# Performance work log

Measured on AMD Instinct MI355X. Metric: run time of the kernel, lower is better.

## Reference

```python
import jax, jax.numpy as jnp
import numpy as np

N_HEAD = 16
HEAD_DIM = 64
EPS_RMS = 1e-6


def _rope(x, cos, sin):
    # x: [B, T, H, D]; cos/sin: [T, D//2] broadcast to [1, T, 1, D//2]
    d2 = x.shape[-1] // 2
    x1, x2 = x[..., :d2], x[..., d2:]
    c = cos[None, :, None, :]
    s = sin[None, :, None, :]
    return jnp.concatenate([x1 * c + x2 * s, -x1 * s + x2 * c], axis=-1)


def _rms_norm(x):
    return x * jax.lax.rsqrt(jnp.mean(x * x, axis=-1, keepdims=True) + EPS_RMS)


def setup_inputs() -> dict:
    key = jax.random.key(0)
    ks = jax.random.split(key, 7)
    B, T, C = 1, 4096, 1024
    x = jax.random.normal(ks[0], (B, T, C), dtype=jnp.float32)
    # realistic rotary angles
    d2 = HEAD_DIM // 2
    inv_freq = 1.0 / (10000.0 ** (np.arange(0, d2, dtype=np.float32) / d2))
    ang = np.arange(T, dtype=np.float32)[:, None] * inv_freq[None, :]
    cos = jnp.asarray(np.cos(ang), dtype=jnp.float32)
    sin = jnp.asarray(np.sin(ang), dtype=jnp.float32)
    scale = 0.02
    wq = jax.random.normal(ks[1], (C, C), dtype=jnp.float32) * scale
    wk = jax.random.normal(ks[2], (C, C), dtype=jnp.float32) * scale
    wv = jax.random.normal(ks[3], (C, C), dtype=jnp.float32) * scale
    wproj = jax.random.normal(ks[4], (C, C), dtype=jnp.float32) * scale
    return {"x": x, "cos": cos, "sin": sin, "wq": wq, "wk": wk, "wv": wv, "wproj": wproj}


def reference(x, cos, sin, wq, wk, wv, wproj):
    B, T, C = x.shape
    H, D = N_HEAD, HEAD_DIM
    # QKV projections (torch Linear: x @ W.T)
    q = (x @ wq.T).reshape(B, T, H, D)
    k = (x @ wk.T).reshape(B, T, H, D)
    v = (x @ wv.T).reshape(B, T, H, D)
    # RoPE then QK RMS-norm
    q = _rms_norm(_rope(q, cos, sin))
    k = _rms_norm(_rope(k, cos, sin))
    # [B, H, T, D]
    q = q.transpose(0, 2, 1, 3)
    k = k.transpose(0, 2, 1, 3)
    v = v.transpose(0, 2, 1, 3)
    scores = jnp.einsum('bhqd,bhkd->bhqk', q, k) * (1.0 / D ** 0.5)
    # causal mask (kv_cache is None, Tq == Tk == T)
    mask = jnp.tril(jnp.ones((T, T), dtype=bool))
    scores = jnp.where(mask[None, None, :, :], scores, -jnp.inf)
    attn = jax.nn.sigmoid(scores)  # sigmoid(-inf) == 0
    y = jnp.einsum('bhqk,bhkd->bhqd', attn, v)
    y = y / (T ** 0.5 + 1e-6)
    y = y.transpose(0, 2, 1, 3).reshape(B, T, C)
    return y @ wproj.T
```

## Files before the change

### kernel.cpp

```cpp
#include <hip/hip_runtime.h>

typedef __attribute__((ext_vector_type(8))) short bf16x8;
typedef __attribute__((ext_vector_type(4))) float f32x4;
typedef __attribute__((ext_vector_type(16))) float f32x16;

__device__ inline f32x4 mfma16(bf16x8 a, bf16x8 b, f32x4 c) {
    return __builtin_amdgcn_mfma_f32_16x16x32_bf16(a, b, c, 0, 0, 0);
}
__device__ inline f32x16 mfma32(bf16x8 a, bf16x8 b, f32x16 c) {
    return __builtin_amdgcn_mfma_f32_32x32x16_bf16(a, b, c, 0, 0, 0);
}

__device__ inline short f2bf(float f) {
    unsigned u = __builtin_bit_cast(unsigned, f);
    unsigned r = (u + 0x7fffu + ((u >> 16) & 1u)) >> 16;
    return (short)r;
}
__device__ inline float bf2f(short h) {
    unsigned u = ((unsigned)(unsigned short)h) << 16;
    return __builtin_bit_cast(float, u);
}

__device__ inline unsigned cvt_pk_bf16(float lo, float hi) {
    unsigned r;
    asm("v_cvt_pk_bf16_f32 %0, %1, %2" : "=v"(r) : "v"(lo), "v"(hi));
    return r;
}
__device__ inline void plane_swap(unsigned& a, unsigned& b) {
    asm("v_permlane32_swap_b32 %0, %1" : "+v"(a), "+v"(b));
}
__device__ inline float exp2_hw(float x) {
    float r;
    asm("v_exp_f32 %0, %1" : "=v"(r) : "v"(x));
    return r;
}

#define GAS(p) (const __attribute__((address_space(1))) void*)(p)
#define LAS(p) (__attribute__((address_space(3))) void*)(p)

#define T_SEQ 4096
#define C_DIM 1024
#define N_HEAD 16
#define HEAD_DIM 64
#define QSCALE (-0.18033688011112042f)
#define INV64 (1.0f / (64.0f + 1e-6f))

__global__ __launch_bounds__(256) void cast5(
    const float* __restrict__ s0, const float* __restrict__ s1,
    const float* __restrict__ s2, const float* __restrict__ s3,
    const float* __restrict__ s4,
    short* __restrict__ d0, short* __restrict__ d1, short* __restrict__ d2,
    short* __restrict__ d3, short* __restrict__ d4,
    int n0, int n1, int n2, int n3, int n4)
{
    int z = blockIdx.y;
    const float* s; short* d; int n;
    switch (z) {
        case 0: s = s0; d = d0; n = n0; break;
        case 1: s = s1; d = d1; n = n1; break;
        case 2: s = s2; d = d2; n = n2; break;
        case 3: s = s3; d = d3; n = n3; break;
        default: s = s4; d = d4; n = n4; break;
    }
    float sc = (z == 4) ? INV64 : 1.0f;
    int i = (blockIdx.x * 256 + threadIdx.x) * 4;
    if (i >= n) return;
    float4 v = *(const float4*)&s[i];
    short4 o;
    o.x = f2bf(v.x * sc); o.y = f2bf(v.y * sc);
    o.z = f2bf(v.z * sc); o.w = f2bf(v.w * sc);
    *(short4*)&d[i] = o;
}

#define QSTAGE(t_, b_) do {                                                      \
    int k0_ = (t_) * 32;                                                         \
    _Pragma("unroll")                                                            \
    for (int s2_ = 0; s2_ < 2; s2_++) {                                          \
        int rbase_ = wave * 32 + s2_ * 16;                                       \
        __builtin_amdgcn_global_load_lds(                                        \
            GAS(&A[(size_t)(row0 + rbase_ + srow) * KK + k0_ + scolx]),          \
            LAS(&sA[b_][rbase_ * 32]), 16, 0, 0);                                \
        __builtin_amdgcn_global_load_lds(                                        \
            GAS(&B[(size_t)(col0 + rbase_ + srow) * KK + k0_ + scolx]),          \
            LAS(&sB[b_][rbase_ * 32]), 16, 0, 0);                                \
    }                                                                            \
} while (0)

#define GEMM_STEP2(t_, nt_, bcur_) do {                                          \
    if ((t_) + 1 < (nt_)) {                                                      \
        QSTAGE((t_) + 1, (bcur_) ^ 1);                                           \
        asm volatile("s_waitcnt vmcnt(4)" ::: "memory");                         \
    } else {                                                                     \
        asm volatile("s_waitcnt vmcnt(0)" ::: "memory");                         \
    }                                                                            \
    __builtin_amdgcn_s_barrier();                                                \
    bf16x8 af[4], bfv[4];                                                        \
    _Pragma("unroll")                                                            \
    for (int m = 0; m < 4; m++) {                                                \
        int row_ = wr * 64 + m * 16 + llo;                                       \
        af[m] = *(const bf16x8*)&sA[bcur_][row_ * 32 + ((lhi ^ (llo & 3)) * 8)]; \
    }                                                                            \
    _Pragma("unroll")                                                            \
    for (int n = 0; n < 4; n++) {                                                \
        int row_ = wc * 64 + n * 16 + llo;                                       \
        bfv[n] = *(const bf16x8*)&sB[bcur_][row_ * 32 + ((lhi ^ (llo & 3)) * 8)];\
    }                                                                            \
    __builtin_amdgcn_s_setprio(1);                                               \
    _Pragma("unroll")                                                            \
    for (int m = 0; m < 4; m++)                                                  \
        _Pragma("unroll")                                                        \
        for (int n = 0; n < 4; n++)                                              \
            acc[m][n] = mfma16(af[m], bfv[n], acc[m][n]);                        \
    __builtin_amdgcn_s_setprio(0);                                               \
    asm volatile("" ::: "memory");                                               \
    __builtin_amdgcn_s_barrier();                                                \
} while (0)

__global__ __launch_bounds__(256, 4) void gemm_qkv(
    const short* __restrict__ A,
    const short* __restrict__ B0, const short* __restrict__ B1,
    const short* __restrict__ B2,
    short* __restrict__ qnb, short* __restrict__ knb, short* __restrict__ vtb,
    const float* __restrict__ cosT, const float* __restrict__ sinT)
{
    int xx = blockIdx.x;
    int ct = xx & 7, z = xx >> 3;
    const short* B = (z == 0) ? B0 : ((z == 1) ? B1 : B2);

    __shared__ alignas(16) short sA[2][128 * 32];
    __shared__ alignas(16) short sB[2][128 * 32];

    int tid  = threadIdx.x;
    int wave = tid >> 6, lane = tid & 63;
    int lhi  = lane >> 4, llo = lane & 15;
    int wr   = wave >> 1, wc = wave & 1;
    int row0 = blockIdx.y * 128, col0 = ct * 128;
    const int KK = C_DIM;

    int srow  = lane >> 2;
    int scolx = (((lane & 3) ^ (srow & 3)) * 8);

    f32x4 acc[4][4];
#pragma unroll
    for (int m = 0; m < 4; m++)
#pragma unroll
        for (int n = 0; n < 4; n++)
            acc[m][n] = (f32x4){0.f, 0.f, 0.f, 0.f};

    QSTAGE(0, 0);
    int bcur = 0;
    for (int t = 0; t < 32; t++) {
        GEMM_STEP2(t, 32, bcur);
        bcur ^= 1;
    }

    int hH = ct * 2 + wc;
    if (z < 2) {
        short* dst = z ? knb : qnb;
        float osc = z ? 1.0f : QSCALE;
#pragma unroll
        for (int m = 0; m < 4; m++)
#pragma unroll
            for (int r = 0; r < 4; r++) {
                int row = row0 + wr * 64 + m * 16 + lhi * 4 + r;
                float c0 = cosT[row * 32 + llo],      c1 = cosT[row * 32 + 16 + llo];
                float s0 = sinT[row * 32 + llo],      s1 = sinT[row * 32 + 16 + llo];
                float e0 = acc[m][0][r], e1 = acc[m][1][r];
                float e2 = acc[m][2][r], e3 = acc[m][3][r];
                float r0 = e0 * c0 + e2 * s0;
                float r1 = e1 * c1 + e3 * s1;
                float r2 = e2 * c0 - e0 * s0;
                float r3 = e3 * c1 - e1 * s1;
                float sq = r0 * r0 + r1 * r1 + r2 * r2 + r3 * r3;
                sq += __shfl_xor(sq, 1);
                sq += __shfl_xor(sq, 2);
                sq += __shfl_xor(sq, 4);
                sq += __shfl_xor(sq, 8);
                float inv = rsqrtf(sq * (1.0f / 64.0f) + 1e-6f) * osc;
                size_t base = ((size_t)hH * T_SEQ + row) * HEAD_DIM + llo;
                dst[base +  0] = f2bf(r0 * inv);
                dst[base + 16] = f2bf(r1 * inv);
                dst[base + 32] = f2bf(r2 * inv);
                dst[base + 48] = f2bf(r3 * inv);
            }
    } else {
#pragma unroll
        for (int m = 0; m < 4; m++)
#pragma unroll
            for (int n = 0; n < 4; n++) {
                int trow = row0 + wr * 64 + m * 16 + lhi * 4;
                short4 o;
                o.x = f2bf(acc[m][n][0]);
                o.y = f2bf(acc[m][n][1]);
                o.z = f2bf(acc[m][n][2]);
                o.w = f2bf(acc[m][n][3]);
                *(short4*)&vtb[((size_t)(hH * HEAD_DIM + n * 16 + llo)) * T_SEQ + trow] = o;
            }
    }
}

__global__ __launch_bounds__(256, 4) void gemm_proj(
    const short* __restrict__ A, const short* __restrict__ B,
    float* __restrict__ C, int M, int N, int K)
{
    __shared__ alignas(16) short sA[2][128 * 32];
    __shared__ alignas(16) short sB[2][128 * 32];

    int tid  = threadIdx.x;
    int wave = tid >> 6, lane = tid & 63;
    int lhi  = lane >> 4, llo = lane & 15;
    int wr   = wave >> 1, wc = wave & 1;
    int row0 = blockIdx.y * 128, col0 = blockIdx.x * 128;
    const int KK = K;

    int srow  = lane >> 2;
    int scolx = (((lane & 3) ^ (srow & 3)) * 8);

    f32x4 acc[4][4];
#pragma unroll
    for (int m = 0; m < 4; m++)
#pragma unroll
        for (int n = 0; n < 4; n++)
            acc[m][n] = (f32x4){0.f, 0.f, 0.f, 0.f};

    int nt = K >> 5;
    QSTAGE(0, 0);
    int bcur = 0;
    for (int t = 0; t < nt; t++) {
        GEMM_STEP2(t, nt, bcur);
        bcur ^= 1;
    }

#pragma unroll
    for (int m = 0; m < 4; m++)
#pragma unroll
        for (int n = 0; n < 4; n++)
#pragma unroll
            for (int r = 0; r < 4; r++) {
                int row = row0 + wr * 64 + m * 16 + lhi * 4 + r;
                int col = col0 + wc * 64 + n * 16 + llo;
                C[(size_t)row * N + col] = acc[m][n][r];
            }
}

#define STAGE6(s_, bf_) do {                                                     \
    int kb_ = (s_) * 64;                                                         \
    int r_  = lane >> 3;                                                         \
    int ss_ = (lane & 7) ^ r_;                                                   \
    __builtin_amdgcn_global_load_lds(                                            \
        GAS(Kh + (size_t)(kb_ + wv * 16 + r_) * HEAD_DIM + ss_ * 8),             \
        LAS(Smem + (bf_) * 8192 + (wv * 16) * 128), 16, 0, 0);                   \
    __builtin_amdgcn_global_load_lds(                                            \
        GAS(Kh + (size_t)(kb_ + wv * 16 + 8 + r_) * HEAD_DIM + ss_ * 8),         \
        LAS(Smem + (bf_) * 8192 + (wv * 16 + 8) * 128), 16, 0, 0);               \
    __builtin_amdgcn_global_load_lds(                                            \
        GAS(Vh + (size_t)(wv * 16 + r_) * T_SEQ + kb_ + ss_ * 8),                \
        LAS(Smem + 16384 + (bf_) * 8192 + (wv * 16) * 128), 16, 0, 0);           \
    __builtin_amdgcn_global_load_lds(                                            \
        GAS(Vh + (size_t)(wv * 16 + 8 + r_) * T_SEQ + kb_ + ss_ * 8),            \
        LAS(Smem + 16384 + (bf_) * 8192 + (wv * 16 + 8) * 128), 16, 0, 0);       \
} while (0)

__global__ __launch_bounds__(256, 4) void attn6(
    const short* __restrict__ qn, const short* __restrict__ kn,
    const short* __restrict__ vt, short* __restrict__ yb)
{
    __shared__ alignas(16) char Smem[32768];

    int id = blockIdx.x;
    int h  = id & 15;
    int g  = id >> 4;
    int t  = (g < 16) ? (63 - g) : (g < 32) ? (g - 16)
           : (g < 48) ? (79 - g) : (g - 32);
    int ns = t + 1;

    int tid = threadIdx.x, wv = tid >> 6, lane = tid & 63;
    int lo = lane & 31, hi = lane >> 5;
    int band = wv & 1, tm = wv >> 1;

    const short* Qh = qn + (size_t)h * T_SEQ * HEAD_DIM;
    const short* Kh = kn + (size_t)h * T_SEQ * HEAD_DIM;
    const short* Vh = vt + (size_t)h * HEAD_DIM * T_SEQ;

    int q0 = t * 64;
    int qrow  = q0 + band * 32 + lo;
    int qmaxw = q0 + band * 32 + 31;

    const short* Qr = &Qh[(size_t)qrow * HEAD_DIM + hi * 8];
    bf16x8 qf0 = *(const bf16x8*)&Qr[0];
    bf16x8 qf1 = *(const bf16x8*)&Qr[16];
    bf16x8 qf2 = *(const bf16x8*)&Qr[32];
    bf16x8 qf3 = *(const bf16x8*)&Qr[48];

    f32x16 zed;
#pragma unroll
    for (int r = 0; r < 16; r++) zed[r] = 0.f;

    f32x16 yac0, yac1;
#pragma unroll
    for (int r = 0; r < 16; r++) { yac0[r] = 0.f; yac1[r] = 0.f; }

    unsigned sw   = (unsigned)((lo & 7) << 4);
    unsigned krow = (unsigned)((tm * 32 + lo) * 128);
    unsigned ko0 = krow + ((0u * 32 + hi * 16) ^ sw);
    unsigned ko1 = krow + ((1u * 32 + hi * 16) ^ sw);
    unsigned ko2 = krow + ((2u * 32 + hi * 16) ^ sw);
    unsigned ko3 = krow + ((3u * 32 + hi * 16) ^ sw);
    unsigned vrow0 = (unsigned)(lo * 128)        + 16384u;
    unsigned vrow1 = (unsigned)((32 + lo) * 128) + 16384u;
    unsigned vo00 = vrow0 + (((unsigned)(tm * 64 + 0 * 32 + hi * 16)) ^ sw);
    unsigned vo01 = vrow0 + (((unsigned)(tm * 64 + 1 * 32 + hi * 16)) ^ sw);
    unsigned vo10 = vrow1 + (((unsigned)(tm * 64 + 0 * 32 + hi * 16)) ^ sw);
    unsigned vo11 = vrow1 + (((unsigned)(tm * 64 + 1 * 32 + hi * 16)) ^ sw);

    STAGE6(0, 0);
    int buf = 0;
    for (int s = 0; s < ns; s++) {
        if (s + 1 < ns) {
            STAGE6(s + 1, buf ^ 1);
            asm volatile("s_waitcnt vmcnt(4)" ::: "memory");
        } else {
            asm volatile("s_waitcnt vmcnt(0)" ::: "memory");
        }
        __builtin_amdgcn_s_barrier();

        int kb0 = s * 64 + tm * 32;
        if (kb0 <= qmaxw) {
            const char* B_ = Smem + (buf << 13);
            bf16x8 kf0 = *(const bf16x8*)(B_ + ko0);
            bf16x8 kf1 = *(const bf16x8*)(B_ + ko1);
            bf16x8 kf2 = *(const bf16x8*)(B_ + ko2);
            bf16x8 kf3 = *(const bf16x8*)(B_ + ko3);
            bf16x8 vf00 = *(const bf16x8*)(B_ + vo00);
            bf16x8 vf01 = *(const bf16x8*)(B_ + vo01);
            bf16x8 vf10 = *(const bf16x8*)(B_ + vo10);
            bf16x8 vf11 = *(const bf16x8*)(B_ + vo11);

            f32x16 sv;
            __builtin_amdgcn_s_setprio(1);
            sv = mfma32(kf0, qf0, zed);
            sv = mfma32(kf1, qf1, sv);
            sv = mfma32(kf2, qf2, sv);
            sv = mfma32(kf3, qf3, sv);
            __builtin_amdgcn_s_setprio(0);

            if (kb0 + 31 > q0 + band * 32) {
#pragma unroll
                for (int r = 0; r < 16; r++) {
                    int kvg = kb0 + (r & 3) + 8 * (r >> 2) + 4 * hi;
                    float pv = __builtin_amdgcn_rcpf(1.f + exp2_hw(sv[r]));
                    sv[r] = (kvg <= qrow) ? pv : 0.f;
                }
            } else {
#pragma unroll
                for (int r = 0; r < 16; r++)
                    sv[r] = __builtin_amdgcn_rcpf(1.f + exp2_hw(sv[r]));
            }

#pragma unroll
            for (int k2 = 0; k2 < 2; k2++) {
                unsigned wA = cvt_pk_bf16(sv[8 * k2 + 0], sv[8 * k2 + 1]);
                unsigned wC = cvt_pk_bf16(sv[8 * k2 + 2], sv[8 * k2 + 3]);
                unsigned wB = cvt_pk_bf16(sv[8 * k2 + 4], sv[8 * k2 + 5]);
                unsigned wD = cvt_pk_bf16(sv[8 * k2 + 6], sv[8 * k2 + 7]);
                plane_swap(wA, wB);
                plane_swap(wC, wD);
                union { unsigned u[4]; bf16x8 v; } pw;
                pw.u[0] = wA; pw.u[1] = wC; pw.u[2] = wB; pw.u[3] = wD;
                __builtin_amdgcn_s_setprio(1);
                yac0 = mfma32(pw.v, k2 ? vf01 : vf00, yac0);
                yac1 = mfma32(pw.v, k2 ? vf11 : vf10, yac1);
                __builtin_amdgcn_s_setprio(0);
            }
        }
        asm volatile("" ::: "memory");
        __builtin_amdgcn_s_barrier();
        buf ^= 1;
    }

    __syncthreads();
    float* Yred = (float*)Smem;
    if (tm == 1) {
#pragma unroll
        for (int d = 0; d < 2; d++)
#pragma unroll
            for (int r = 0; r < 16; r++) {
                int crow = (r & 3) + 8 * (r >> 2) + 4 * hi;
                Yred[(band * 32 + crow) * 64 + d * 32 + lo] = d ? yac1[r] : yac0[r];
            }
    }
    __syncthreads();
    if (tm == 0) {
#pragma unroll
        for (int d = 0; d < 2; d++)
#pragma unroll
            for (int r = 0; r < 16; r++) {
                int crow = (r & 3) + 8 * (r >> 2) + 4 * hi;
                float v = (d ? yac1[r] : yac0[r]) + Yred[(band * 32 + crow) * 64 + d * 32 + lo];
                yb[(size_t)(q0 + band * 32 + crow) * C_DIM + h * HEAD_DIM + d * 32 + lo] = f2bf(v);
            }
    }
}

extern "C" void kernel_launch(void* const* d_in, const int* in_sizes, int n_in,
                              void* d_out, int out_size, void* d_ws, size_t ws_size,
                              hipStream_t stream)
{
    const float* x    = (const float*)d_in[0];
    const float* cosT = (const float*)d_in[1];
    const float* sinT = (const float*)d_in[2];
    const float* wq   = (const float*)d_in[3];
    const float* wk   = (const float*)d_in[4];
    const float* wv   = (const float*)d_in[5];
    const float* wp   = (const float*)d_in[6];

    char* ws = (char*)d_ws;
    const size_t MB = 1024 * 1024;
    short* xb    = (short*)(ws + 0);
    short* wqb   = (short*)(ws + 8  * MB);
    short* wkb   = (short*)(ws + 10 * MB);
    short* wvb   = (short*)(ws + 12 * MB);
    short* wpb   = (short*)(ws + 14 * MB);
    short* qnb   = (short*)(ws + 16 * MB);
    short* knb   = (short*)(ws + 24 * MB);
    short* vtb   = (short*)(ws + 32 * MB);
    short* yb    = (short*)(ws + 40 * MB);

    cast5<<<dim3(4096, 5, 1), 256, 0, stream>>>(
        x, wq, wk, wv, wp, xb, wqb, wkb, wvb, wpb,
        T_SEQ * C_DIM, C_DIM * C_DIM, C_DIM * C_DIM, C_DIM * C_DIM, C_DIM * C_DIM);

    gemm_qkv<<<dim3(24, 32, 1), 256, 0, stream>>>(
        xb, wqb, wkb, wvb, qnb, knb, vtb, cosT, sinT);

    attn6<<<1024, 256, 0, stream>>>(qnb, knb, vtb, yb);

    gemm_proj<<<dim3(8, 32, 1), 256, 0, stream>>>(
        yb, wpb, (float*)d_out, T_SEQ, C_DIM, C_DIM);
}
```

Before: 129.1 us.

## Triple-buffer K/V tiles in attention with one barrier per step

Moves the attention kernel's K/V staging from a double buffer to a triple buffer, prefetching two tiles ahead and unrolling the loop three times with fixed buffer indices. This lets each step use a single barrier instead of two. The goal is to hide more global-load latency and cut synchronisation cost. In exchange LDS per block grows to 48KB and the occupancy bound drops from 4 to 3 blocks per CU.

```diff
diff --git a/kernel.cpp b/kernel.cpp
--- a/kernel.cpp
+++ b/kernel.cpp
@@ -243,7 +243,8 @@
             }
 }
 
-#define STAGE6(s_, bf_) do {                                                     \
+
+#define STAGE20(s_, bf_) do {                                                    \
     int kb_ = (s_) * 64;                                                         \
     int r_  = lane >> 3;                                                         \
     int ss_ = (lane & 7) ^ r_;                                                   \
@@ -255,17 +256,70 @@
         LAS(Smem + (bf_) * 8192 + (wv * 16 + 8) * 128), 16, 0, 0);               \
     __builtin_amdgcn_global_load_lds(                                            \
         GAS(Vh + (size_t)(wv * 16 + r_) * T_SEQ + kb_ + ss_ * 8),                \
-        LAS(Smem + 16384 + (bf_) * 8192 + (wv * 16) * 128), 16, 0, 0);           \
+        LAS(Smem + 24576 + (bf_) * 8192 + (wv * 16) * 128), 16, 0, 0);           \
     __builtin_amdgcn_global_load_lds(                                            \
         GAS(Vh + (size_t)(wv * 16 + 8 + r_) * T_SEQ + kb_ + ss_ * 8),            \
-        LAS(Smem + 16384 + (bf_) * 8192 + (wv * 16 + 8) * 128), 16, 0, 0);       \
+        LAS(Smem + 24576 + (bf_) * 8192 + (wv * 16 + 8) * 128), 16, 0, 0);       \
 } while (0)
 
-__global__ __launch_bounds__(256, 4) void attn6(
+#define ASTEP(b_, bn_) {                                                         \
+    if (s + 1 < ns) { asm volatile("s_waitcnt vmcnt(8)" ::: "memory"); }         \
+    else            { asm volatile("s_waitcnt vmcnt(0)" ::: "memory"); }         \
+    __builtin_amdgcn_s_barrier();                                                \
+    if (s + 2 < ns) STAGE20(s + 2, bn_);                                         \
+    int kb0 = s * 64 + tm * 32;                                                  \
+    if (kb0 <= qmaxw) {                                                          \
+        const char* KB_ = Smem + (b_) * 8192;                                    \
+        const char* VB_ = Smem + 24576 + (b_) * 8192;                            \
+        bf16x8 kf0 = *(const bf16x8*)(KB_ + ko0);                                \
+        bf16x8 kf1 = *(const bf16x8*)(KB_ + ko1);                                \
+        bf16x8 kf2 = *(const bf16x8*)(KB_ + ko2);                                \
+        bf16x8 kf3 = *(const bf16x8*)(KB_ + ko3);                                \
+        bf16x8 vf00 = *(const bf16x8*)(VB_ + vo00);                              \
+        bf16x8 vf01 = *(const bf16x8*)(VB_ + vo01);                              \
+        bf16x8 vf10 = *(const bf16x8*)(VB_ + vo10);                              \
+        bf16x8 vf11 = *(const bf16x8*)(VB_ + vo11);                              \
+        f32x16 sv;                                                               \
+        __builtin_amdgcn_s_setprio(1);                                           \
+        sv = mfma32(kf0, qf0, zed);                                              \
+        sv = mfma32(kf1, qf1, sv);                                               \
+        sv = mfma32(kf2, qf2, sv);                                               \
+        sv = mfma32(kf3, qf3, sv);                                               \
+        __builtin_amdgcn_s_setprio(0);                                           \
+        if (kb0 + 31 > qminw) {                                                  \
+            _Pragma("unroll") for (int r = 0; r < 16; r++) {                     \
+                int kvg = kb0 + (r & 3) + 8 * (r >> 2) + 4 * hi;                 \
+                float pv = __builtin_amdgcn_rcpf(1.f + exp2_hw(sv[r]));          \
+                sv[r] = (kvg <= qrow) ? pv : 0.f;                                \
+            }                                                                    \
+        } else {                                                                 \
+            _Pragma("unroll") for (int r = 0; r < 16; r++)                       \
+                sv[r] = __builtin_amdgcn_rcpf(1.f + exp2_hw(sv[r]));             \
+        }                                                                        \
+        _Pragma("unroll") for (int k2 = 0; k2 < 2; k2++) {                       \
+            unsigned wA = cvt_pk_bf16(sv[8 * k2 + 0], sv[8 * k2 + 1]);           \
+            unsigned wC = cvt_pk_bf16(sv[8 * k2 + 2], sv[8 * k2 + 3]);           \
+            unsigned wB = cvt_pk_bf16(sv[8 * k2 + 4], sv[8 * k2 + 5]);           \
+            unsigned wD = cvt_pk_bf16(sv[8 * k2 + 6], sv[8 * k2 + 7]);           \
+            plane_swap(wA, wB);                                                  \
+            plane_swap(wC, wD);                                                  \
+            union { unsigned u[4]; bf16x8 v; } pw;                               \
+            pw.u[0] = wA; pw.u[1] = wC; pw.u[2] = wB; pw.u[3] = wD;              \
+            __builtin_amdgcn_s_setprio(1);                                       \
+            yac0 = mfma32(pw.v, k2 ? vf01 : vf00, yac0);                         \
+            yac1 = mfma32(pw.v, k2 ? vf11 : vf10, yac1);                         \
+            __builtin_amdgcn_s_setprio(0);                                       \
+        }                                                                        \
+    }                                                                            \
+    asm volatile("" ::: "memory");                                               \
+    if (++s >= ns) goto eplg;                                                    \
+}
+
+__global__ __launch_bounds__(256, 3) void attn20(
     const short* __restrict__ qn, const short* __restrict__ kn,
     const short* __restrict__ vt, short* __restrict__ yb)
 {
-    __shared__ alignas(16) char Smem[32768];
+    __shared__ alignas(16) char Smem[49152];
 
     int id = blockIdx.x;
     int h  = id & 15;
@@ -284,6 +338,7 @@
 
     int q0 = t * 64;
     int qrow  = q0 + band * 32 + lo;
+    int qminw = q0 + band * 32;
     int qmaxw = q0 + band * 32 + 31;
 
     const short* Qr = &Qh[(size_t)qrow * HEAD_DIM + hi * 8];
@@ -306,77 +361,25 @@
     unsigned ko1 = krow + ((1u * 32 + hi * 16) ^ sw);
     unsigned ko2 = krow + ((2u * 32 + hi * 16) ^ sw);
     unsigned ko3 = krow + ((3u * 32 + hi * 16) ^ sw);
-    unsigned vrow0 = (unsigned)(lo * 128)        + 16384u;
-    unsigned vrow1 = (unsigned)((32 + lo) * 128) + 16384u;
+    unsigned vrow0 = (unsigned)(lo * 128);
+    unsigned vrow1 = (unsigned)((32 + lo) * 128);
     unsigned vo00 = vrow0 + (((unsigned)(tm * 64 + 0 * 32 + hi * 16)) ^ sw);
     unsigned vo01 = vrow0 + (((unsigned)(tm * 64 + 1 * 32 + hi * 16)) ^ sw);
     unsigned vo10 = vrow1 + (((unsigned)(tm * 64 + 0 * 32 + hi * 16)) ^ sw);
     unsigned vo11 = vrow1 + (((unsigned)(tm * 64 + 1 * 32 + hi * 16)) ^ sw);
 
-    STAGE6(0, 0);
-    int buf = 0;
-    for (int s = 0; s < ns; s++) {
-        if (s + 1 < ns) {
-            STAGE6(s + 1, buf ^ 1);
-            asm volatile("s_waitcnt vmcnt(4)" ::: "memory");
-        } else {
-            asm volatile("s_waitcnt vmcnt(0)" ::: "memory");
+    STAGE20(0, 0);
+    STAGE20(1, 1);
+
+    {
+        int s = 0;
+        while (true) {
+            ASTEP(0, 2);
+            ASTEP(1, 0);
+            ASTEP(2, 1);
         }
-        __builtin_amdgcn_s_barrier();
-
-        int kb0 = s * 64 + tm * 32;
-        if (kb0 <= qmaxw) {
-            const char* B_ = Smem + (buf << 13);
-            bf16x8 kf0 = *(const bf16x8*)(B_ + ko0);
-            bf16x8 kf1 = *(const bf16x8*)(B_ + ko1);
-            bf16x8 kf2 = *(const bf16x8*)(B_ + ko2);
-            bf16x8 kf3 = *(const bf16x8*)(B_ + ko3);
-            bf16x8 vf00 = *(const bf16x8*)(B_ + vo00);
-            bf16x8 vf01 = *(const bf16x8*)(B_ + vo01);
-            bf16x8 vf10 = *(const bf16x8*)(B_ + vo10);
-            bf16x8 vf11 = *(const bf16x8*)(B_ + vo11);
-
-            f32x16 sv;
-            __builtin_amdgcn_s_setprio(1);
-            sv = mfma32(kf0, qf0, zed);
-            sv = mfma32(kf1, qf1, sv);
-            sv = mfma32(kf2, qf2, sv);
-            sv = mfma32(kf3, qf3, sv);
-            __builtin_amdgcn_s_setprio(0);
-
-            if (kb0 + 31 > q0 + band * 32) {
-#pragma unroll
-                for (int r = 0; r < 16; r++) {
-                    int kvg = kb0 + (r & 3) + 8 * (r >> 2) + 4 * hi;
-                    float pv = __builtin_amdgcn_rcpf(1.f + exp2_hw(sv[r]));
-                    sv[r] = (kvg <= qrow) ? pv : 0.f;
-                }
-            } else {
-#pragma unroll
-                for (int r = 0; r < 16; r++)
-                    sv[r] = __builtin_amdgcn_rcpf(1.f + exp2_hw(sv[r]));
-            }
-
-#pragma unroll
-            for (int k2 = 0; k2 < 2; k2++) {
-                unsigned wA = cvt_pk_bf16(sv[8 * k2 + 0], sv[8 * k2 + 1]);
-                unsigned wC = cvt_pk_bf16(sv[8 * k2 + 2], sv[8 * k2 + 3]);
-                unsigned wB = cvt_pk_bf16(sv[8 * k2 + 4], sv[8 * k2 + 5]);
-                unsigned wD = cvt_pk_bf16(sv[8 * k2 + 6], sv[8 * k2 + 7]);
-                plane_swap(wA, wB);
-                plane_swap(wC, wD);
-                union { unsigned u[4]; bf16x8 v; } pw;
-                pw.u[0] = wA; pw.u[1] = wC; pw.u[2] = wB; pw.u[3] = wD;
-                __builtin_amdgcn_s_setprio(1);
-                yac0 = mfma32(pw.v, k2 ? vf01 : vf00, yac0);
-                yac1 = mfma32(pw.v, k2 ? vf11 : vf10, yac1);
-                __builtin_amdgcn_s_setprio(0);
-            }
-        }
-        asm volatile("" ::: "memory");
-        __builtin_amdgcn_s_barrier();
-        buf ^= 1;
-    }
+    }
+eplg:
 
     __syncthreads();
     float* Yred = (float*)Smem;
@@ -433,7 +436,7 @@
     gemm_qkv<<<dim3(24, 32, 1), 256, 0, stream>>>(
         xb, wqb, wkb, wvb, qnb, knb, vtb, cosT, sinT);
 
-    attn6<<<1024, 256, 0, stream>>>(qnb, knb, vtb, yb);
+    attn20<<<1024, 256, 0, stream>>>(qnb, knb, vtb, yb);
 
     gemm_proj<<<dim3(8, 32, 1), 256, 0, stream>>>(
         yb, wpb, (float*)d_out, T_SEQ, C_DIM, C_DIM);
```

Result: no change. 128.9 us (-0.1%).
